# Optimization experiments

Measured on AMD Instinct MI355X. Metric: run time of the kernel, lower is better.

The kernel has to match this reference:

```python
import jax, jax.numpy as jnp
import numpy as np


def _pair_indices(attention_mask, special_tokens_mask):
    # Mirror get_aa_pair_indices: use sample 0, keep non-pad, non-special positions,
    # then take upper-triangle (offset=1) pairs. Masks are constants -> numpy ok.
    am = np.asarray(attention_mask)
    sm = np.asarray(special_tokens_mask)
    aa_mask = (am[0] == 1) & (sm[0] == 0)
    aa_positions = np.nonzero(aa_mask)[0]
    n_aa = aa_positions.shape[0]
    if n_aa < 2:
        e = np.zeros(0, dtype=np.int64)
        return e, e
    tri_i, tri_j = np.triu_indices(n_aa, k=1)
    return aa_positions[tri_i], aa_positions[tri_j]


def setup_inputs() -> dict:
    key = jax.random.key(0)
    k1, k2, k3 = jax.random.split(key, 3)
    B, L, H = 2, 512, 512
    hidden_states = jax.random.normal(k1, (B, L, H), dtype=jnp.float32)
    W = jax.random.normal(k2, (1, H, H), dtype=jnp.float32) / np.sqrt(H)
    b = jax.random.normal(k3, (1,), dtype=jnp.float32)
    attention_mask = jnp.ones((B, L), dtype=jnp.int32)
    special_tokens_mask = jnp.zeros((B, L), dtype=jnp.int32)
    return {
        "hidden_states": hidden_states,
        "W": W,
        "b": b,
        "attention_mask": attention_mask,
        "special_tokens_mask": special_tokens_mask,
    }


def reference(hidden_states, W, b, attention_mask, special_tokens_mask):
    # Dropout is identity at inference time.
    idx_i, idx_j = _pair_indices(attention_mask, special_tokens_mask)
    if idx_i.size == 0:
        return jnp.zeros((hidden_states.shape[0], 0), dtype=hidden_states.dtype)
    h_i = hidden_states[:, idx_i]  # (B, P, H) — large gathered intermediate
    h_j = hidden_states[:, idx_j]  # (B, P, H)
    # nn.Bilinear with out_features=1: out[b,p] = h_i[b,p] @ W[0] @ h_j[b,p] + b[0]
    logits = jnp.einsum("bph,hk,bpk->bp", h_i, W[0], h_j) + b[0]
    return logits
```

## Files before the change

kernel.cpp:

```cpp
#include <hip/hip_runtime.h>


#define LSEQ 512
#define HDIM 512
#define NPAIR 130816
#define KT 32
#define PADA 36
#define PADH 68
#define GELEMS (2 * LSEQ * HDIM)
#define PSTRIDE (2 * NPAIR)

__global__ __launch_bounds__(128)
void gemm_g(const float* __restrict__ hid, const float* __restrict__ W,
            float* __restrict__ G4) {
    __shared__ float As[KT][PADA];
    __shared__ float Bs[KT][64];
    const int b  = blockIdx.z >> 2;
    const int s  = blockIdx.z & 3;
    const int m0 = blockIdx.y * 32;
    const int n0 = blockIdx.x * 64;
    const int t  = threadIdx.x;
    const int tx = t & 15, ty = t >> 4;
    const float* A = hid + b * (LSEQ * HDIM);

    float acc[4][4] = {};
    for (int k0 = s * 128; k0 < s * 128 + 128; k0 += KT) {
        #pragma unroll
        for (int l = 0; l < 2; ++l) {
            const int idx = t + l * 128;
            const int r = idx >> 3, c4 = (idx & 7) << 2;
            float4 va = *(const float4*)&A[(m0 + r) * HDIM + k0 + c4];
            As[c4 + 0][r] = va.x; As[c4 + 1][r] = va.y;
            As[c4 + 2][r] = va.z; As[c4 + 3][r] = va.w;
        }
        #pragma unroll
        for (int l = 0; l < 4; ++l) {
            const int idx = t + l * 128;
            const int r = idx >> 4, c4 = (idx & 15) << 2;
            *(float4*)&Bs[r][c4] = *(const float4*)&W[(k0 + r) * HDIM + n0 + c4];
        }
        __syncthreads();
        #pragma unroll
        for (int kk = 0; kk < KT; ++kk) {
            const float4 av = *(const float4*)&As[kk][ty << 2];
            const float4 bv = *(const float4*)&Bs[kk][tx << 2];
            const float a[4] = {av.x, av.y, av.z, av.w};
            const float w4[4] = {bv.x, bv.y, bv.z, bv.w};
            #pragma unroll
            for (int i = 0; i < 4; ++i)
                #pragma unroll
                for (int j = 0; j < 4; ++j)
                    acc[i][j] += a[i] * w4[j];
        }
        __syncthreads();
    }
    float* Gp = G4 + s * GELEMS + b * (LSEQ * HDIM);
    #pragma unroll
    for (int i = 0; i < 4; ++i)
        *(float4*)&Gp[(m0 + (ty << 2) + i) * HDIM + n0 + (tx << 2)] =
            make_float4(acc[i][0], acc[i][1], acc[i][2], acc[i][3]);
}

__global__ __launch_bounds__(256)
void pair(const float* __restrict__ G4, const float* __restrict__ hid,
          float* __restrict__ P) {
    __shared__ float Gs[KT][PADA];
    __shared__ float Hs[KT][PADH];
    const int b = blockIdx.y;
    const int s = blockIdx.z;
    int rem = blockIdx.x, bi = 0;
    while (rem >= 8 - (bi >> 1)) { rem -= 8 - (bi >> 1); ++bi; }
    const int bj = (bi >> 1) + rem;
    const int i0 = bi * 32, j0 = bj * 64;
    const int t  = threadIdx.x;
    const int tx = t & 15, ty = t >> 4;
    const float* Gb0 = G4 + 0 * GELEMS + b * (LSEQ * HDIM);
    const float* Gb1 = G4 + 1 * GELEMS + b * (LSEQ * HDIM);
    const float* Gb2 = G4 + 2 * GELEMS + b * (LSEQ * HDIM);
    const float* Gb3 = G4 + 3 * GELEMS + b * (LSEQ * HDIM);
    const float* Hb  = hid + b * (LSEQ * HDIM);

    float acc[2][4] = {};
    for (int k0 = s * 128; k0 < s * 128 + 128; k0 += KT) {
        {
            const int r = t >> 3, c4 = (t & 7) << 2;
            const int off = (i0 + r) * HDIM + k0 + c4;
            float4 v0 = *(const float4*)&Gb0[off];
            float4 v1 = *(const float4*)&Gb1[off];
            float4 v2 = *(const float4*)&Gb2[off];
            float4 v3 = *(const float4*)&Gb3[off];
            Gs[c4 + 0][r] = (v0.x + v1.x) + (v2.x + v3.x);
            Gs[c4 + 1][r] = (v0.y + v1.y) + (v2.y + v3.y);
            Gs[c4 + 2][r] = (v0.z + v1.z) + (v2.z + v3.z);
            Gs[c4 + 3][r] = (v0.w + v1.w) + (v2.w + v3.w);
        }
        #pragma unroll
        for (int l = 0; l < 2; ++l) {
            const int idx = t + l * 256;
            const int r = idx >> 3, c4 = (idx & 7) << 2;
            float4 vh = *(const float4*)&Hb[(j0 + r) * HDIM + k0 + c4];
            Hs[c4 + 0][r] = vh.x; Hs[c4 + 1][r] = vh.y;
            Hs[c4 + 2][r] = vh.z; Hs[c4 + 3][r] = vh.w;
        }
        __syncthreads();
        #pragma unroll
        for (int kk = 0; kk < KT; ++kk) {
            const float2 gv = *(const float2*)&Gs[kk][ty << 1];
            const float4 hv = *(const float4*)&Hs[kk][tx << 2];
            const float g[2] = {gv.x, gv.y};
            const float h[4] = {hv.x, hv.y, hv.z, hv.w};
            #pragma unroll
            for (int i = 0; i < 2; ++i)
                #pragma unroll
                for (int j = 0; j < 4; ++j)
                    acc[i][j] += g[i] * h[j];
        }
        __syncthreads();
    }

    float* Pp = P + s * PSTRIDE + b * NPAIR;
    #pragma unroll
    for (int ii = 0; ii < 2; ++ii) {
        const int i = i0 + (ty << 1) + ii;
        const int rowbase = (i * (1023 - i)) >> 1;
        const int jb = j0 + (tx << 2);
        #pragma unroll
        for (int jj = 0; jj < 4; ++jj) {
            const int j = jb + jj;
            if (j > i) Pp[rowbase + j - i - 1] = acc[ii][jj];
        }
    }
}

__global__ __launch_bounds__(256)
void reduce_bias(const float* __restrict__ P, const float* __restrict__ bias,
                 float* __restrict__ out) {
    const int i = blockIdx.x * 256 + threadIdx.x;
    const int n4 = PSTRIDE / 4;
    if (i < n4) {
        const float4* P4 = (const float4*)P;
        float4 v0 = P4[i];
        float4 v1 = P4[i + 1 * n4];
        float4 v2 = P4[i + 2 * n4];
        float4 v3 = P4[i + 3 * n4];
        const float bb = bias[0];
        float4 r;
        r.x = (v0.x + v1.x) + (v2.x + v3.x) + bb;
        r.y = (v0.y + v1.y) + (v2.y + v3.y) + bb;
        r.z = (v0.z + v1.z) + (v2.z + v3.z) + bb;
        r.w = (v0.w + v1.w) + (v2.w + v3.w) + bb;
        ((float4*)out)[i] = r;
    }
}

extern "C" void kernel_launch(void* const* d_in, const int* in_sizes, int n_in,
                              void* d_out, int out_size, void* d_ws, size_t ws_size,
                              hipStream_t stream) {
    const float* hid  = (const float*)d_in[0];
    const float* W    = (const float*)d_in[1];
    const float* bias = (const float*)d_in[2];
    float* out = (float*)d_out;
    float* G4  = (float*)d_ws;
    float* P   = (float*)d_ws + 4 * GELEMS;

    gemm_g<<<dim3(8, 16, 8), 128, 0, stream>>>(hid, W, G4);
    pair<<<dim3(72, 2, 4), 256, 0, stream>>>(G4, hid, P);
    reduce_bias<<<256, 256, 0, stream>>>(P, bias, out);
}
```

Measured before the change: 89.38 us.

## Compute hidden@W GEMM with bf16x3 split MFMA instead of FP32 FMA

Replaces the scalar FP32 tiled GEMM for G = hid·W with a kernel using MFMA 16x16x32 bf16 instructions. Each FP32 value is split into high and low bf16 parts, and three cross products are accumulated to approximate FP32 accuracy. Tiles grow to 64x64 per 256-thread block, with the split done while staging data into LDS. This trades some precision, plus the extra split arithmetic and LDS traffic, for matrix-core throughput on the first stage.

```diff
diff --git a/kernel.cpp b/kernel.cpp
--- a/kernel.cpp
+++ b/kernel.cpp
@@ -7,58 +7,101 @@
 #define KT 32
 #define PADA 36
 #define PADH 68
+#define LDSP 40
 #define GELEMS (2 * LSEQ * HDIM)
 #define PSTRIDE (2 * NPAIR)
 
-__global__ __launch_bounds__(128)
-void gemm_g(const float* __restrict__ hid, const float* __restrict__ W,
-            float* __restrict__ G4) {
-    __shared__ float As[KT][PADA];
-    __shared__ float Bs[KT][64];
+typedef __attribute__((ext_vector_type(8))) short bf16x8;
+typedef __attribute__((ext_vector_type(4))) short bf16x4;
+typedef __attribute__((ext_vector_type(4))) float f32x4;
+
+__device__ __forceinline__ void split2(float f, short& hi, short& lo) {
+    unsigned u = __float_as_uint(f);
+    hi = (short)(u >> 16);
+    float hif = __uint_as_float(u & 0xffff0000u);
+    lo = (short)(__float_as_uint(f - hif) >> 16);
+}
+
+__global__ __launch_bounds__(256)
+void gemm_mfma(const float* __restrict__ hid, const float* __restrict__ W,
+               float* __restrict__ G4) {
+    __shared__ short Ah[64][LDSP], Al[64][LDSP];
+    __shared__ short Bh[64][LDSP], Bl[64][LDSP];
     const int b  = blockIdx.z >> 2;
     const int s  = blockIdx.z & 3;
-    const int m0 = blockIdx.y * 32;
+    const int m0 = blockIdx.y * 64;
     const int n0 = blockIdx.x * 64;
-    const int t  = threadIdx.x;
-    const int tx = t & 15, ty = t >> 4;
+    const int t    = threadIdx.x;
+    const int lane = t & 63, w = t >> 6;
+    const int wm = w >> 1, wn = w & 1;
     const float* A = hid + b * (LSEQ * HDIM);
 
-    float acc[4][4] = {};
+    f32x4 acc00 = {}, acc01 = {}, acc10 = {}, acc11 = {};
+
     for (int k0 = s * 128; k0 < s * 128 + 128; k0 += KT) {
         #pragma unroll
         for (int l = 0; l < 2; ++l) {
-            const int idx = t + l * 128;
+            const int idx = t + l * 256;
             const int r = idx >> 3, c4 = (idx & 7) << 2;
-            float4 va = *(const float4*)&A[(m0 + r) * HDIM + k0 + c4];
-            As[c4 + 0][r] = va.x; As[c4 + 1][r] = va.y;
-            As[c4 + 2][r] = va.z; As[c4 + 3][r] = va.w;
-        }
-        #pragma unroll
-        for (int l = 0; l < 4; ++l) {
-            const int idx = t + l * 128;
-            const int r = idx >> 4, c4 = (idx & 15) << 2;
-            *(float4*)&Bs[r][c4] = *(const float4*)&W[(k0 + r) * HDIM + n0 + c4];
-        }
-        __syncthreads();
-        #pragma unroll
-        for (int kk = 0; kk < KT; ++kk) {
-            const float4 av = *(const float4*)&As[kk][ty << 2];
-            const float4 bv = *(const float4*)&Bs[kk][tx << 2];
-            const float a[4] = {av.x, av.y, av.z, av.w};
-            const float w4[4] = {bv.x, bv.y, bv.z, bv.w};
-            #pragma unroll
-            for (int i = 0; i < 4; ++i)
-                #pragma unroll
-                for (int j = 0; j < 4; ++j)
-                    acc[i][j] += a[i] * w4[j];
-        }
-        __syncthreads();
-    }
+            float4 v = *(const float4*)&A[(m0 + r) * HDIM + k0 + c4];
+            short h0, h1, h2, h3, l0, l1, l2, l3;
+            split2(v.x, h0, l0); split2(v.y, h1, l1);
+            split2(v.z, h2, l2); split2(v.w, h3, l3);
+            *(bf16x4*)&Ah[r][c4] = (bf16x4){h0, h1, h2, h3};
+            *(bf16x4*)&Al[r][c4] = (bf16x4){l0, l1, l2, l3};
+        }
+        #pragma unroll
+        for (int l = 0; l < 2; ++l) {
+            const int idx = t + l * 256;
+            const int kr = idx >> 4, c4 = (idx & 15) << 2;
+            float4 v = *(const float4*)&W[(k0 + kr) * HDIM + n0 + c4];
+            short h, lo;
+            split2(v.x, h, lo); Bh[c4 + 0][kr] = h; Bl[c4 + 0][kr] = lo;
+            split2(v.y, h, lo); Bh[c4 + 1][kr] = h; Bl[c4 + 1][kr] = lo;
+            split2(v.z, h, lo); Bh[c4 + 2][kr] = h; Bl[c4 + 2][kr] = lo;
+            split2(v.w, h, lo); Bh[c4 + 3][kr] = h; Bl[c4 + 3][kr] = lo;
+        }
+        __syncthreads();
+
+        const int fr   = lane & 15;
+        const int koff = (lane >> 4) << 3;
+        bf16x8 ah0 = *(const bf16x8*)&Ah[wm * 32 + fr     ][koff];
+        bf16x8 ah1 = *(const bf16x8*)&Ah[wm * 32 + 16 + fr][koff];
+        bf16x8 al0 = *(const bf16x8*)&Al[wm * 32 + fr     ][koff];
+        bf16x8 al1 = *(const bf16x8*)&Al[wm * 32 + 16 + fr][koff];
+        bf16x8 bh0 = *(const bf16x8*)&Bh[wn * 32 + fr     ][koff];
+        bf16x8 bh1 = *(const bf16x8*)&Bh[wn * 32 + 16 + fr][koff];
+        bf16x8 bl0 = *(const bf16x8*)&Bl[wn * 32 + fr     ][koff];
+        bf16x8 bl1 = *(const bf16x8*)&Bl[wn * 32 + 16 + fr][koff];
+
+        acc00 = __builtin_amdgcn_mfma_f32_16x16x32_bf16(ah0, bh0, acc00, 0, 0, 0);
+        acc01 = __builtin_amdgcn_mfma_f32_16x16x32_bf16(ah0, bh1, acc01, 0, 0, 0);
+        acc10 = __builtin_amdgcn_mfma_f32_16x16x32_bf16(ah1, bh0, acc10, 0, 0, 0);
+        acc11 = __builtin_amdgcn_mfma_f32_16x16x32_bf16(ah1, bh1, acc11, 0, 0, 0);
+        acc00 = __builtin_amdgcn_mfma_f32_16x16x32_bf16(ah0, bl0, acc00, 0, 0, 0);
+        acc01 = __builtin_amdgcn_mfma_f32_16x16x32_bf16(ah0, bl1, acc01, 0, 0, 0);
+        acc10 = __builtin_amdgcn_mfma_f32_16x16x32_bf16(ah1, bl0, acc10, 0, 0, 0);
+        acc11 = __builtin_amdgcn_mfma_f32_16x16x32_bf16(ah1, bl1, acc11, 0, 0, 0);
+        acc00 = __builtin_amdgcn_mfma_f32_16x16x32_bf16(al0, bh0, acc00, 0, 0, 0);
+        acc01 = __builtin_amdgcn_mfma_f32_16x16x32_bf16(al0, bh1, acc01, 0, 0, 0);
+        acc10 = __builtin_amdgcn_mfma_f32_16x16x32_bf16(al1, bh0, acc10, 0, 0, 0);
+        acc11 = __builtin_amdgcn_mfma_f32_16x16x32_bf16(al1, bh1, acc11, 0, 0, 0);
+
+        __syncthreads();
+    }
+
     float* Gp = G4 + s * GELEMS + b * (LSEQ * HDIM);
+    const int drow = (lane >> 4) << 2;
+    const int dcol = lane & 15;
     #pragma unroll
-    for (int i = 0; i < 4; ++i)
-        *(float4*)&Gp[(m0 + (ty << 2) + i) * HDIM + n0 + (tx << 2)] =
-            make_float4(acc[i][0], acc[i][1], acc[i][2], acc[i][3]);
+    for (int r = 0; r < 4; ++r) {
+        const int row0 = m0 + wm * 32 + drow + r;
+        const int col0 = n0 + wn * 32 + dcol;
+        Gp[(row0     ) * HDIM + col0     ] = acc00[r];
+        Gp[(row0     ) * HDIM + col0 + 16] = acc01[r];
+        Gp[(row0 + 16) * HDIM + col0     ] = acc10[r];
+        Gp[(row0 + 16) * HDIM + col0 + 16] = acc11[r];
+    }
 }
 
 __global__ __launch_bounds__(256)
@@ -163,7 +206,7 @@
     float* G4  = (float*)d_ws;
     float* P   = (float*)d_ws + 4 * GELEMS;
 
-    gemm_g<<<dim3(8, 16, 8), 128, 0, stream>>>(hid, W, G4);
+    gemm_mfma<<<dim3(8, 8, 8), 256, 0, stream>>>(hid, W, G4);
     pair<<<dim3(72, 2, 4), 256, 0, stream>>>(G4, hid, P);
     reduce_bias<<<256, 256, 0, stream>>>(P, bias, out);
 }
```

New measurement: 87.44 us. 2.2% less time.
